# Kernel optimization log

Hardware: AMD Instinct MI355X
Metric: run time of the kernel (lower is better)

The kernel has to match this reference:

```python
import jax, jax.numpy as jnp
import numpy as np


def _box_probs(box):
    """box: [B, P, s, s] binary float. Returns [B, s*s] normalized histogram of
    per-patch popcounts, matching tf.math.bincount(minlength=1, maxlength=s*s)
    semantics (values == s*s are dropped), then /P, then row-normalized."""
    B, P, s, _ = box.shape
    s2 = s * s
    sums = jnp.sum(box, axis=(2, 3)).astype(jnp.int32)  # [B, P] popcounts in [0, s2]
    # per-row bincount of length s2 via one-hot compare (drops value == s2, as TF does)
    bins = jnp.arange(s2, dtype=jnp.int32)
    counts = jnp.sum(sums[:, :, None] == bins[None, None, :], axis=1).astype(jnp.float32)  # [B, s2]
    probs = counts / jnp.float32(P)
    probs = probs / jnp.sum(probs, axis=1, keepdims=True)
    return probs


def setup_inputs() -> dict:
    key = jax.random.key(0)
    ks = jax.random.split(key, 4)
    B, P = 16, 32768
    mk = lambda k, s: jax.random.randint(k, (B, P, s, s), 0, 2).astype(jnp.float32)
    return {
        "cd0_box0": mk(ks[0], 4),
        "cd0_box1": mk(ks[1], 8),
        "cd1_box0": mk(ks[2], 4),
        "cd1_box1": mk(ks[3], 8),
    }


def reference(cd0_box0, cd0_box1, cd1_box0, cd1_box1):
    # nested-list output in the original -> flat tuple here, same order:
    # [[cd0_box0, cd0_box1], [cd1_box0, cd1_box1]]
    return (
        _box_probs(cd0_box0),  # [16, 16]
        _box_probs(cd0_box1),  # [16, 64]
        _box_probs(cd1_box0),  # [16, 16]
        _box_probs(cd1_box1),  # [16, 64]
    )
```

## Files before the change

kernel.cpp:

```cpp
#include <hip/hip_runtime.h>


#define P_PATCH 32768
#define B_ROWS  16
#define NPATCH  (B_ROWS * P_PATCH)

template <int S2, int VEC>
__device__ __forceinline__ void hist_box(const float4* __restrict__ in,
                                         int* __restrict__ gcounts,
                                         int block_rank, int num_blocks,
                                         int* lds) {
    for (int i = threadIdx.x; i < B_ROWS * S2; i += 256) lds[i] = 0;
    __syncthreads();

    const int nthreads = num_blocks * 256;
    for (int g = block_rank * 256 + (int)threadIdx.x; g < NPATCH; g += nthreads) {
        const float4* p = in + (size_t)g * VEC;
        float s = 0.f;
#pragma unroll
        for (int j = 0; j < VEC; ++j) {
            float4 v = p[j];
            s += (v.x + v.y) + (v.z + v.w);
        }
        int bin = (int)(s + 0.5f);
        int b = g >> 15;
        if (bin < S2)
            atomicAdd(&lds[b * S2 + bin], 1);
    }
    __syncthreads();

    for (int i = threadIdx.x; i < B_ROWS * S2; i += 256) {
        int c = lds[i];
        if (c) atomicAdd(&gcounts[i], c);
    }
}

__global__ __launch_bounds__(256) void hist_kernel(const float4* __restrict__ in0,
                                                   const float4* __restrict__ in1,
                                                   const float4* __restrict__ in2,
                                                   const float4* __restrict__ in3,
                                                   int* __restrict__ ws) {
    __shared__ int lds[B_ROWS * 64];
    const int bid = blockIdx.x;
    if (bid < 128)      hist_box<16, 4 >(in0, ws + 0,    bid,       128, lds);
    else if (bid < 640) hist_box<64, 16>(in1, ws + 256,  bid - 128, 512, lds);
    else if (bid < 768) hist_box<16, 4 >(in2, ws + 1280, bid - 640, 128, lds);
    else                hist_box<64, 16>(in3, ws + 1536, bid - 768, 512, lds);
}

__global__ __launch_bounds__(64) void norm_kernel(const int* __restrict__ ws,
                                                  float* __restrict__ out) {
    const int row  = blockIdx.x;
    const int lane = threadIdx.x;
    const int box  = row >> 4;
    const int r    = row & 15;
    const int bins = (box & 1) ? 64 : 16;
    int off = (box == 0) ? 0 : (box == 1) ? 256 : (box == 2) ? 1280 : 1536;
    off += r * bins;

    int c = (lane < bins) ? ws[off + lane] : 0;
    int total = c;
#pragma unroll
    for (int d = 32; d > 0; d >>= 1) total += __shfl_down(total, d);
    total = __shfl(total, 0);

    if (lane < bins) out[off + lane] = (float)c / (float)total;
}

extern "C" void kernel_launch(void* const* d_in, const int* in_sizes, int n_in,
                              void* d_out, int out_size, void* d_ws, size_t ws_size,
                              hipStream_t stream) {
    const float4* in0 = (const float4*)d_in[0];
    const float4* in1 = (const float4*)d_in[1];
    const float4* in2 = (const float4*)d_in[2];
    const float4* in3 = (const float4*)d_in[3];
    int* ws = (int*)d_ws;

    hipMemsetAsync(ws, 0, 2560 * sizeof(int), stream);
    hist_kernel<<<1280, 256, 0, stream>>>(in0, in1, in2, in3, ws);
    norm_kernel<<<64, 64, 0, stream>>>(ws, (float*)d_out);
}
```

Measured before the change: 325.7 us.

## Coalesce histogram loads with lane-group shuffle reduction and more blocks

Each patch's float4 values are now spread across a group of adjacent lanes, so consecutive threads read consecutive float4s instead of each thread striding through a whole patch. Per-patch sums are combined with xor shuffles, and four loads are issued before any reduction to raise memory-level parallelism. The grid grows from 1280 to 3840 blocks to cover the bandwidth-bound 640 MB read. Costs are the extra shuffle instructions and more blocks each flushing their LDS histogram to global atomics.

```diff
diff --git a/kernel.cpp b/kernel.cpp
--- a/kernel.cpp
+++ b/kernel.cpp
@@ -5,27 +5,40 @@
 #define B_ROWS  16
 #define NPATCH  (B_ROWS * P_PATCH)
 
-template <int S2, int VEC>
+template <int FV, int LOG2FV>
 __device__ __forceinline__ void hist_box(const float4* __restrict__ in,
                                          int* __restrict__ gcounts,
                                          int block_rank, int num_blocks,
                                          int* lds) {
+    constexpr int S2 = FV * 4;
+    constexpr int U  = 4;
+    const int N4     = NPATCH * FV;
+    const int ntiles = N4 / (256 * U);
+
     for (int i = threadIdx.x; i < B_ROWS * S2; i += 256) lds[i] = 0;
     __syncthreads();
 
-    const int nthreads = num_blocks * 256;
-    for (int g = block_rank * 256 + (int)threadIdx.x; g < NPATCH; g += nthreads) {
-        const float4* p = in + (size_t)g * VEC;
-        float s = 0.f;
+    const int lane_grp = threadIdx.x & (FV - 1);
+
+    for (int t = block_rank; t < ntiles; t += num_blocks) {
+        const int base = t * (256 * U) + (int)threadIdx.x;
+        float4 v[U];
 #pragma unroll
-        for (int j = 0; j < VEC; ++j) {
-            float4 v = p[j];
-            s += (v.x + v.y) + (v.z + v.w);
+        for (int k = 0; k < U; ++k) v[k] = in[base + k * 256];
+#pragma unroll
+        for (int k = 0; k < U; ++k) {
+            float s = (v[k].x + v[k].y) + (v[k].z + v[k].w);
+#pragma unroll
+            for (int off = 1; off < FV; off <<= 1) s += __shfl_xor(s, off);
+            if (lane_grp == 0) {
+                const int q     = base + k * 256;
+                const int patch = q >> LOG2FV;
+                const int row   = patch >> 15;
+                const int bin   = (int)(s + 0.5f);
+                if (bin < S2)
+                    atomicAdd(&lds[row * S2 + bin], 1);
+            }
         }
-        int bin = (int)(s + 0.5f);
-        int b = g >> 15;
-        if (bin < S2)
-            atomicAdd(&lds[b * S2 + bin], 1);
     }
     __syncthreads();
 
@@ -35,6 +48,9 @@
     }
 }
 
+#define NB0 384
+#define NB1 1536
+
 __global__ __launch_bounds__(256) void hist_kernel(const float4* __restrict__ in0,
                                                    const float4* __restrict__ in1,
                                                    const float4* __restrict__ in2,
@@ -42,10 +58,10 @@
                                                    int* __restrict__ ws) {
     __shared__ int lds[B_ROWS * 64];
     const int bid = blockIdx.x;
-    if (bid < 128)      hist_box<16, 4 >(in0, ws + 0,    bid,       128, lds);
-    else if (bid < 640) hist_box<64, 16>(in1, ws + 256,  bid - 128, 512, lds);
-    else if (bid < 768) hist_box<16, 4 >(in2, ws + 1280, bid - 640, 128, lds);
-    else                hist_box<64, 16>(in3, ws + 1536, bid - 768, 512, lds);
+    if (bid < NB0)                  hist_box<4, 2>(in0, ws + 0,    bid,                 NB0, lds);
+    else if (bid < NB0 + NB1)       hist_box<16,4>(in1, ws + 256,  bid - NB0,           NB1, lds);
+    else if (bid < 2*NB0 + NB1)     hist_box<4, 2>(in2, ws + 1280, bid - NB0 - NB1,     NB0, lds);
+    else                            hist_box<16,4>(in3, ws + 1536, bid - 2*NB0 - NB1,   NB1, lds);
 }
 
 __global__ __launch_bounds__(64) void norm_kernel(const int* __restrict__ ws,
@@ -77,6 +93,6 @@
     int* ws = (int*)d_ws;
 
     hipMemsetAsync(ws, 0, 2560 * sizeof(int), stream);
-    hist_kernel<<<1280, 256, 0, stream>>>(in0, in1, in2, in3, ws);
+    hist_kernel<<<2 * (NB0 + NB1), 256, 0, stream>>>(in0, in1, in2, in3, ws);
     norm_kernel<<<64, 64, 0, stream>>>(ws, (float*)d_out);
 }
```

Result: no change. 319.8 us (-1.8%).

## Stream patches into LDS via async global_load_lds ring with DPP reductions

Applied to the files above, without the earlier changes.

Each wave now loads contiguous 2KB chunks of one batch row straight into a 4-deep LDS ring buffer with global_load_lds, using explicit vmcnt waits so loads overlap compute. Per-patch sums are formed cooperatively across lanes with DPP shuffles instead of each thread reading its own strided patch. Histograms become per-wave, one row per block, and the block count for the 8x8 inputs drops from 512 to 384. The goal is fully coalesced, deeper in-flight memory traffic on this bandwidth-bound read. The cost is hand-written waitcnt logic that depends on how the compiler orders memory instructions, plus fewer blocks in flight.

```diff
diff --git a/kernel.cpp b/kernel.cpp
--- a/kernel.cpp
+++ b/kernel.cpp
@@ -3,49 +3,122 @@
 
 #define P_PATCH 32768
 #define B_ROWS  16
-#define NPATCH  (B_ROWS * P_PATCH)
 
-template <int S2, int VEC>
+template <int CTRL>
+__device__ __forceinline__ float dpp_add(float s) {
+    int t = __builtin_amdgcn_update_dpp(0, __float_as_int(s), CTRL, 0xF, 0xF, true);
+    return s + __int_as_float(t);
+}
+
+__device__ __forceinline__ void dma1k(const float4* g, float4* l) {
+    __builtin_amdgcn_global_load_lds((const __attribute__((address_space(1))) void*)g,
+                                     (__attribute__((address_space(3))) void*)l,
+                                     16, 0, 0);
+}
+
+template <int FV>
 __device__ __forceinline__ void hist_box(const float4* __restrict__ in,
                                          int* __restrict__ gcounts,
-                                         int block_rank, int num_blocks,
-                                         int* lds) {
-    for (int i = threadIdx.x; i < B_ROWS * S2; i += 256) lds[i] = 0;
+                                         int block_rank, int blocks_per_box,
+                                         float4* ring_all, int* hist) {
+    constexpr int S2  = FV * 4;
+    constexpr int HP  = S2 + 1;
+    constexpr int D   = 4;
+    constexpr int TF4 = 128;
+
+    const int tid  = (int)threadIdx.x;
+    const int lane = tid & 63;
+    const int wid  = tid >> 6;
+
+    const int bpr    = blocks_per_box >> 4;
+    const int row    = block_rank / bpr;
+    const int wr     = (block_rank % bpr) * 4 + wid;
+    const int stride = bpr * 4;
+    const int TPR    = (P_PATCH * FV) / TF4;
+    const float4* rowbase = in + (size_t)row * (P_PATCH * FV);
+
+    float4* ring = ring_all + wid * (D * TF4);
+    int*    h    = hist + wid * HP;
+
+    for (int b = tid; b < 4 * HP; b += 256) hist[b] = 0;
     __syncthreads();
 
-    const int nthreads = num_blocks * 256;
-    for (int g = block_rank * 256 + (int)threadIdx.x; g < NPATCH; g += nthreads) {
-        const float4* p = in + (size_t)g * VEC;
-        float s = 0.f;
+    const int niter = (TPR - wr + stride - 1) / stride;
+
 #pragma unroll
-        for (int j = 0; j < VEC; ++j) {
-            float4 v = p[j];
-            s += (v.x + v.y) + (v.z + v.w);
+    for (int d = 0; d < D; ++d) {
+        if (d < niter) {
+            const float4* g = rowbase + (size_t)(wr + d * stride) * TF4 + lane;
+            float4* l = ring + d * TF4 + lane;
+            dma1k(g, l);
+            dma1k(g + 64, l + 64);
         }
-        int bin = (int)(s + 0.5f);
-        int b = g >> 15;
-        if (bin < S2)
-            atomicAdd(&lds[b * S2 + bin], 1);
+    }
+
+    int slot = 0;
+    for (int i = 0; i < niter; ++i) {
+        const int R = (niter - i < D) ? (niter - i) : D;
+        switch (R) {
+            case 4:  asm volatile("s_waitcnt vmcnt(6)" ::: "memory"); break;
+            case 3:  asm volatile("s_waitcnt vmcnt(4)" ::: "memory"); break;
+            case 2:  asm volatile("s_waitcnt vmcnt(2)" ::: "memory"); break;
+            default: asm volatile("s_waitcnt vmcnt(0)" ::: "memory"); break;
+        }
+
+        float4* l = ring + slot * TF4;
+        float s01[2];
+#pragma unroll
+        for (int k = 0; k < 2; ++k) {
+            float4 v = l[k * 64 + lane];
+            float x = (v.x + v.y) + (v.z + v.w);
+            x = dpp_add<0xB1>(x);
+            x = dpp_add<0x4E>(x);
+            if (FV == 16) {
+                x = dpp_add<0x124>(x);
+                x = dpp_add<0x128>(x);
+            }
+            s01[k] = x;
+        }
+
+        if ((lane & (FV - 1)) == 0) {
+#pragma unroll
+            for (int k = 0; k < 2; ++k) {
+                int b = (int)(s01[k] + 0.5f);
+                if (b < S2) atomicAdd(&h[b], 1);
+            }
+        }
+
+        if (i + D < niter) {
+            const float4* g = rowbase + (size_t)(wr + (i + D) * stride) * TF4 + lane;
+            float4* ld = ring + slot * TF4 + lane;
+            dma1k(g, ld);
+            dma1k(g + 64, ld + 64);
+        }
+        slot = (slot + 1) & (D - 1);
     }
     __syncthreads();
 
-    for (int i = threadIdx.x; i < B_ROWS * S2; i += 256) {
-        int c = lds[i];
-        if (c) atomicAdd(&gcounts[i], c);
+    for (int b = tid; b < S2; b += 256) {
+        int c = hist[b] + hist[HP + b] + hist[2 * HP + b] + hist[3 * HP + b];
+        if (c) atomicAdd(&gcounts[row * S2 + b], c);
     }
 }
 
-__global__ __launch_bounds__(256) void hist_kernel(const float4* __restrict__ in0,
-                                                   const float4* __restrict__ in1,
-                                                   const float4* __restrict__ in2,
-                                                   const float4* __restrict__ in3,
-                                                   int* __restrict__ ws) {
-    __shared__ int lds[B_ROWS * 64];
+#define NB0 128
+#define NB1 384
+
+__global__ __launch_bounds__(256, 4) void hist_kernel(const float4* __restrict__ in0,
+                                                      const float4* __restrict__ in1,
+                                                      const float4* __restrict__ in2,
+                                                      const float4* __restrict__ in3,
+                                                      int* __restrict__ ws) {
+    __shared__ float4 ring[4 * 4 * 128];
+    __shared__ int    hist[4 * 65];
     const int bid = blockIdx.x;
-    if (bid < 128)      hist_box<16, 4 >(in0, ws + 0,    bid,       128, lds);
-    else if (bid < 640) hist_box<64, 16>(in1, ws + 256,  bid - 128, 512, lds);
-    else if (bid < 768) hist_box<16, 4 >(in2, ws + 1280, bid - 640, 128, lds);
-    else                hist_box<64, 16>(in3, ws + 1536, bid - 768, 512, lds);
+    if (bid < NB0)              hist_box<4 >(in0, ws + 0,    bid,               NB0, ring, hist);
+    else if (bid < NB0 + NB1)   hist_box<16>(in1, ws + 256,  bid - NB0,         NB1, ring, hist);
+    else if (bid < 2*NB0 + NB1) hist_box<4 >(in2, ws + 1280, bid - NB0 - NB1,   NB0, ring, hist);
+    else                        hist_box<16>(in3, ws + 1536, bid - 2*NB0 - NB1, NB1, ring, hist);
 }
 
 __global__ __launch_bounds__(64) void norm_kernel(const int* __restrict__ ws,
@@ -77,6 +150,6 @@
     int* ws = (int*)d_ws;
 
     hipMemsetAsync(ws, 0, 2560 * sizeof(int), stream);
-    hist_kernel<<<1280, 256, 0, stream>>>(in0, in1, in2, in3, ws);
+    hist_kernel<<<2 * (NB0 + NB1), 256, 0, stream>>>(in0, in1, in2, in3, ws);
     norm_kernel<<<64, 64, 0, stream>>>(ws, (float*)d_out);
 }
```

Measured after the change: 325.4 us. About the same (-0.1%).

## Coalesce patch loads with DPP lane reductions and packed register histograms

Applied to the files above, without the earlier changes.

Each thread now loads consecutive float4s, so neighbouring lanes read contiguous memory instead of each thread striding through its own whole patch. Per-patch popcounts are reduced across the 4 or 16 lanes holding one patch with DPP swizzles. Each lane keeps a register counter for 4 bins packed as 8-bit fields. Blocks are assigned per batch row, which shrinks LDS to one row's histogram and removes per-patch LDS atomics. The 8-bit packed counters rely on each lane seeing at most 255 hits per bin, which depends on the fixed per-block iteration count.

```diff
diff --git a/kernel.cpp b/kernel.cpp
--- a/kernel.cpp
+++ b/kernel.cpp
@@ -3,49 +3,87 @@
 
 #define P_PATCH 32768
 #define B_ROWS  16
-#define NPATCH  (B_ROWS * P_PATCH)
 
-template <int S2, int VEC>
+template <int CTRL>
+__device__ __forceinline__ float dpp_add(float s) {
+    int t = __builtin_amdgcn_update_dpp(0, __float_as_int(s), CTRL, 0xF, 0xF, true);
+    return s + __int_as_float(t);
+}
+
+template <int FV>
+__device__ __forceinline__ void count_f4(float4 v, int m, unsigned& cnt) {
+    float x = (v.x + v.y) + (v.z + v.w);
+    x = dpp_add<0xB1>(x);
+    x = dpp_add<0x4E>(x);
+    if (FV == 16) {
+        x = dpp_add<0x124>(x);
+        x = dpp_add<0x128>(x);
+    }
+    int bin = (int)(x + 0.5f);
+    cnt += ((bin >> 2) == m) ? (1u << ((bin & 3) << 3)) : 0u;
+}
+
+template <int FV, int BPR>
 __device__ __forceinline__ void hist_box(const float4* __restrict__ in,
                                          int* __restrict__ gcounts,
-                                         int block_rank, int num_blocks,
-                                         int* lds) {
-    for (int i = threadIdx.x; i < B_ROWS * S2; i += 256) lds[i] = 0;
+                                         int block_rank,
+                                         int* ldsHist) {
+    constexpr int S2     = FV * 4;
+    constexpr int U      = 8;
+    constexpr int ROW_F4 = P_PATCH * FV;
+    constexpr int TPR    = ROW_F4 / (256 * U);
+    const int tid = (int)threadIdx.x;
+
+    const int row = block_rank / BPR;
+    const int br  = block_rank % BPR;
+    const float4* rowbase = in + (size_t)row * ROW_F4;
+
+    for (int i = tid; i < S2; i += 256) ldsHist[i] = 0;
     __syncthreads();
 
-    const int nthreads = num_blocks * 256;
-    for (int g = block_rank * 256 + (int)threadIdx.x; g < NPATCH; g += nthreads) {
-        const float4* p = in + (size_t)g * VEC;
-        float s = 0.f;
-#pragma unroll
-        for (int j = 0; j < VEC; ++j) {
-            float4 v = p[j];
-            s += (v.x + v.y) + (v.z + v.w);
-        }
-        int bin = (int)(s + 0.5f);
-        int b = g >> 15;
-        if (bin < S2)
-            atomicAdd(&lds[b * S2 + bin], 1);
+    const int m = tid & (FV - 1);
+    unsigned cnt = 0;
+
+    for (int t = br; t < TPR; t += BPR) {
+        const float4* p = rowbase + t * (256 * U) + tid;
+        float4 v0 = p[0 * 256], v1 = p[1 * 256], v2 = p[2 * 256], v3 = p[3 * 256];
+        float4 v4 = p[4 * 256], v5 = p[5 * 256], v6 = p[6 * 256], v7 = p[7 * 256];
+        count_f4<FV>(v0, m, cnt);
+        count_f4<FV>(v1, m, cnt);
+        count_f4<FV>(v2, m, cnt);
+        count_f4<FV>(v3, m, cnt);
+        count_f4<FV>(v4, m, cnt);
+        count_f4<FV>(v5, m, cnt);
+        count_f4<FV>(v6, m, cnt);
+        count_f4<FV>(v7, m, cnt);
     }
+
+    atomicAdd(&ldsHist[4 * m + 0], (int)( cnt        & 0xffu));
+    atomicAdd(&ldsHist[4 * m + 1], (int)((cnt >>  8) & 0xffu));
+    atomicAdd(&ldsHist[4 * m + 2], (int)((cnt >> 16) & 0xffu));
+    atomicAdd(&ldsHist[4 * m + 3], (int)( cnt >> 24));
     __syncthreads();
 
-    for (int i = threadIdx.x; i < B_ROWS * S2; i += 256) {
-        int c = lds[i];
-        if (c) atomicAdd(&gcounts[i], c);
+    for (int i = tid; i < S2; i += 256) {
+        int c = ldsHist[i];
+        if (c) atomicAdd(&gcounts[row * S2 + i], c);
     }
 }
+
+#define NB0 256
+#define NB1 1024
 
 __global__ __launch_bounds__(256) void hist_kernel(const float4* __restrict__ in0,
                                                    const float4* __restrict__ in1,
                                                    const float4* __restrict__ in2,
                                                    const float4* __restrict__ in3,
                                                    int* __restrict__ ws) {
-    __shared__ int lds[B_ROWS * 64];
+    __shared__ int ldsHist[64];
     const int bid = blockIdx.x;
-    if (bid < 128)      hist_box<16, 4 >(in0, ws + 0,    bid,       128, lds);
-    else if (bid < 640) hist_box<64, 16>(in1, ws + 256,  bid - 128, 512, lds);
-    else if (bid < 768) hist_box<16, 4 >(in2, ws + 1280, bid - 640, 128, lds);
-    else                hist_box<64, 16>(in3, ws + 1536, bid - 768, 512, lds);
+    if (bid < NB0)              hist_box<4,  16>(in0, ws + 0,    bid,               ldsHist);
+    else if (bid < NB0 + NB1)   hist_box<16, 64>(in1, ws + 256,  bid - NB0,         ldsHist);
+    else if (bid < 2*NB0 + NB1) hist_box<4,  16>(in2, ws + 1280, bid - NB0 - NB1,   ldsHist);
+    else                        hist_box<16, 64>(in3, ws + 1536, bid - 2*NB0 - NB1, ldsHist);
 }
 
 __global__ __launch_bounds__(64) void norm_kernel(const int* __restrict__ ws,
@@ -77,6 +115,6 @@
     int* ws = (int*)d_ws;
 
     hipMemsetAsync(ws, 0, 2560 * sizeof(int), stream);
-    hist_kernel<<<1280, 256, 0, stream>>>(in0, in1, in2, in3, ws);
+    hist_kernel<<<2 * (NB0 + NB1), 256, 0, stream>>>(in0, in1, in2, in3, ws);
     norm_kernel<<<64, 64, 0, stream>>>(ws, (float*)d_out);
 }
```

Result: no change. 330.8 us (+1.6%).
